# Kernel optimization log

Hardware: AMD Instinct MI355X
Metric: run time of the kernel (lower is better)

## Reference

```python
import jax, jax.numpy as jnp
import numpy as np

NUM_CLASSES = 80
STRIDES = (8, 16, 32)


def _decode(p, stride):
    # p: [B, 5+C, H, W] raw head -> [B, HW, 5+C] decoded (xy in px, wh=exp*stride)
    B, C, H, W = p.shape
    ys, xs = jnp.meshgrid(jnp.arange(H), jnp.arange(W), indexing='ij')
    grid = jnp.stack([xs, ys], -1).reshape(H * W, 2).astype(p.dtype)
    out = p.reshape(B, C, H * W).transpose(0, 2, 1)
    xy = (out[..., :2] + grid) * stride
    wh = jnp.exp(out[..., 2:4]) * stride
    out = jnp.concatenate([xy, wh, out[..., 4:]], -1)
    es = jnp.full((H * W,), float(stride), p.dtype)
    return out, grid[:, 0], grid[:, 1], es


def _pairwise_iou(gt, pr):
    # gt [G,4] cxcywh, pr [A,4] -> [G,A]
    gt_tl = gt[:, None, :2] - gt[:, None, 2:] * 0.5
    gt_br = gt[:, None, :2] + gt[:, None, 2:] * 0.5
    pr_tl = pr[None, :, :2] - pr[None, :, 2:] * 0.5
    pr_br = pr[None, :, :2] + pr[None, :, 2:] * 0.5
    tl = jnp.maximum(gt_tl, pr_tl)
    br = jnp.minimum(gt_br, pr_br)
    en = jnp.all(tl < br, -1).astype(gt.dtype)
    inter = jnp.prod(br - tl, -1) * en
    a_gt = jnp.prod(gt[:, 2:], -1)[:, None]
    a_pr = jnp.prod(pr[:, 2:], -1)[None, :]
    return inter / (a_gt + a_pr - inter + 1e-16)


def _assign(gt_boxes, gt_cls, bbox, clsp, objp, xg, yg, es):
    # SimOTA assignment for one image (all fixed-shape; non-candidate anchors
    # are masked out via huge cost instead of boolean gather).
    G = gt_boxes.shape[0]
    xc = (xg + 0.5) * es  # [A] anchor centers
    yc = (yg + 0.5) * es
    gl = gt_boxes[:, 0:1] - 0.5 * gt_boxes[:, 2:3]
    gr = gt_boxes[:, 0:1] + 0.5 * gt_boxes[:, 2:3]
    gt_ = gt_boxes[:, 1:2] - 0.5 * gt_boxes[:, 3:4]
    gb = gt_boxes[:, 1:2] + 0.5 * gt_boxes[:, 3:4]
    in_box = (xc[None] > gl) & (xc[None] < gr) & (yc[None] > gt_) & (yc[None] < gb)  # [G,A]
    r = 2.5 * es[None]
    in_ctr = ((xc[None] > gt_boxes[:, 0:1] - r) & (xc[None] < gt_boxes[:, 0:1] + r)
              & (yc[None] > gt_boxes[:, 1:2] - r) & (yc[None] < gt_boxes[:, 1:2] + r))
    fg_cand = jnp.any(in_box, 0) | jnp.any(in_ctr, 0)  # [A]
    in_both = in_box & in_ctr  # [G,A]

    ious = _pairwise_iou(gt_boxes, bbox)  # [G,A]
    ious_m = jnp.where(fg_cand[None, :], ious, 0.0)
    iou_cost = -jnp.log(ious_m + 1e-8)

    # pairwise cls BCE cost: bce(sqrt(sigmoid(cls)*sigmoid(obj)), onehot(gt)).sum(-1)
    p = jnp.sqrt(jax.nn.sigmoid(clsp) * jax.nn.sigmoid(objp[:, None]))  # [A,C]
    lp = jnp.maximum(jnp.log(p), -100.0)
    l1p = jnp.maximum(jnp.log1p(-p), -100.0)
    t = jax.nn.one_hot(gt_cls, NUM_CLASSES, dtype=p.dtype)  # [G,C]
    cls_cost = -(jnp.einsum('ac,gc->ga', lp - l1p, t) + jnp.sum(l1p, -1)[None, :])

    cost = (cls_cost + 3.0 * iou_cost
            + 1e5 * (~in_both).astype(p.dtype)
            + 1e9 * (~fg_cand)[None, :].astype(p.dtype))

    # dynamic-k: k_g = clamp(sum(top10 ious), min=1)
    topk_ious, _ = jax.lax.top_k(ious_m, 10)
    dyn_k = jnp.clip(topk_ious.sum(-1).astype(jnp.int32), 1, None)  # [G]
    rank = jnp.argsort(jnp.argsort(cost, axis=1), axis=1)  # rank of each anchor per gt
    matching = (rank < dyn_k[:, None]) & fg_cand[None, :]  # [G,A]
    # resolve anchors matched to multiple gts: keep min-cost gt
    multi = matching.sum(0) > 1
    best = jnp.argmin(cost, 0)
    matching = jnp.where(multi[None, :], jnp.arange(G)[:, None] == best[None, :], matching)

    fg = jnp.any(matching, 0)  # [A]
    matched_gt = jnp.argmax(matching, 0)  # [A]
    pred_iou = jnp.sum(matching * ious, 0)  # [A]
    matched_cls = gt_cls[matched_gt]
    return fg, matched_gt, pred_iou, matched_cls


def _giou_loss(b, g):
    tl = jnp.maximum(b[..., :2] - b[..., 2:] * 0.5, g[..., :2] - g[..., 2:] * 0.5)
    br = jnp.minimum(b[..., :2] + b[..., 2:] * 0.5, g[..., :2] + g[..., 2:] * 0.5)
    area_b = jnp.prod(b[..., 2:], -1)
    area_g = jnp.prod(g[..., 2:], -1)
    en = jnp.all(tl < br, -1).astype(b.dtype)
    inter = jnp.prod(br - tl, -1) * en
    union = area_b + area_g - inter
    iou = inter / (union + 1e-16)
    ctl = jnp.minimum(b[..., :2] - b[..., 2:] * 0.5, g[..., :2] - g[..., 2:] * 0.5)
    cbr = jnp.maximum(b[..., :2] + b[..., 2:] * 0.5, g[..., :2] + g[..., 2:] * 0.5)
    area_c = jnp.maximum(jnp.prod(cbr - ctl, -1), 1e-16)
    giou = iou - (area_c - union) / area_c
    return 1.0 - jnp.clip(giou, -1.0, 1.0)


def _bce_logits(x, t):
    return jnp.maximum(x, 0.0) - x * t + jnp.log1p(jnp.exp(-jnp.abs(x)))


def _forward(p8, p16, p32, labels):
    outs, xo, yo, eo = [], [], [], []
    for p, s in zip((p8, p16, p32), STRIDES):
        o, x, y, e = _decode(p, s)
        outs.append(o); xo.append(x); yo.append(y); eo.append(e)
    outputs = jnp.concatenate(outs, 1)  # [B, A, 5+C]
    xg = jnp.concatenate(xo); yg = jnp.concatenate(yo); es = jnp.concatenate(eo)

    bbox = outputs[..., :4]
    obj = outputs[..., 4]
    cls = outputs[..., 5:]
    gt_boxes = labels[..., :4]
    gt_cls = labels[..., 4].astype(jnp.int32)

    # assignment runs under no_grad in torch
    det = jax.lax.stop_gradient(outputs)
    fg, matched_gt, pred_iou, matched_cls = jax.vmap(
        lambda gb, gc, o: _assign(gb, gc, o[..., :4], o[..., 5:], o[..., 4], xg, yg, es)
    )(gt_boxes, gt_cls, det)

    fgf = fg.astype(outputs.dtype)  # [B,A]
    reg_t = jnp.take_along_axis(gt_boxes, matched_gt[..., None], axis=1)  # [B,A,4]
    cls_t = (jax.nn.one_hot(matched_cls, NUM_CLASSES, dtype=outputs.dtype)
             * pred_iou[..., None] * fgf[..., None])

    loss_iou = jnp.sum(_giou_loss(bbox, reg_t) * fgf)
    loss_obj = jnp.sum(_bce_logits(obj, fgf))
    loss_cls = jnp.sum(_bce_logits(cls, cls_t) * fgf[..., None])
    num_fg = jnp.maximum(jnp.sum(fgf), 1.0)
    return (5.0 * loss_iou + loss_obj + loss_cls) / num_fg


def setup_inputs() -> dict:
    key = jax.random.key(0)
    k1, k2, k3, k4, k5, k6 = jax.random.split(key, 6)
    B, NGT = 32, 20
    p8 = jax.random.normal(k1, (B, 5 + NUM_CLASSES, 80, 80), dtype=jnp.float32)
    p16 = jax.random.normal(k2, (B, 5 + NUM_CLASSES, 40, 40), dtype=jnp.float32)
    p32 = jax.random.normal(k3, (B, 5 + NUM_CLASSES, 20, 20), dtype=jnp.float32)
    cxy = jax.random.uniform(k4, (B, NGT, 2), dtype=jnp.float32, minval=32.0, maxval=608.0)
    wh = jax.random.uniform(k5, (B, NGT, 2), dtype=jnp.float32, minval=16.0, maxval=128.0)
    cls = jax.random.randint(k6, (B, NGT, 1), 0, NUM_CLASSES).astype(jnp.float32)
    labels = jnp.concatenate([cxy, wh, cls], -1)
    return {"p8": p8, "p16": p16, "p32": p32, "labels": labels}


def reference(p8, p16, p32, labels):
    return _forward(p8, p16, p32, labels)
```

## Files before the change

### kernel.cpp

```cpp
#include <hip/hip_runtime.h>
#include <cstdint>
#include <cstddef>

#define NA 8400
#define NAP 8448
#define NB 32
#define NG 20
#define NCL 80

__device__ __forceinline__ float frcp(float x) { return __builtin_amdgcn_rcpf(x); }
__device__ __forceinline__ float sigm(float x) { return frcp(1.0f + __expf(-x)); }
__device__ __forceinline__ float bce0(float x) {
  return fmaxf(x, 0.0f) + __logf(1.0f + __expf(-fabsf(x)));
}

__device__ __forceinline__ const float* anchor_base(const float* p8, const float* p16,
                                                    const float* p32, int b, int a,
                                                    int& hw, int& HW) {
  if (a < 6400)      { hw = a;        HW = 6400; return p8  + (size_t)b * 85 * 6400; }
  else if (a < 8000) { hw = a - 6400; HW = 1600; return p16 + (size_t)b * 85 * 1600; }
  hw = a - 8000; HW = 400; return p32 + (size_t)b * 85 * 400;
}

__device__ __forceinline__ float iou_raw(float gx, float gy, float gw, float gh, float4 p) {
  float gtlx = gx - gw * 0.5f, gtly = gy - gh * 0.5f;
  float gbrx = gx + gw * 0.5f, gbry = gy + gh * 0.5f;
  float ptlx = p.x - p.z * 0.5f, ptly = p.y - p.w * 0.5f;
  float pbrx = p.x + p.z * 0.5f, pbry = p.y + p.w * 0.5f;
  float tlx = fmaxf(gtlx, ptlx), tly = fmaxf(gtly, ptly);
  float brx = fminf(gbrx, pbrx), bry = fminf(gbry, pbry);
  float inter = ((tlx < brx) && (tly < bry)) ? (brx - tlx) * (bry - tly) : 0.0f;
  float ag = gw * gh, ap = p.z * p.w;
  return inter * frcp(ag + ap - inter + 1e-16f);
}

__device__ __forceinline__ float giou_loss(float4 bb, float gx, float gy, float gw, float gh) {
  float btlx = bb.x - bb.z * 0.5f, btly = bb.y - bb.w * 0.5f;
  float bbrx = bb.x + bb.z * 0.5f, bbry = bb.y + bb.w * 0.5f;
  float gtlx = gx - gw * 0.5f, gtly = gy - gh * 0.5f;
  float gbrx = gx + gw * 0.5f, gbry = gy + gh * 0.5f;
  float tlx = fmaxf(btlx, gtlx), tly = fmaxf(btly, gtly);
  float brx = fminf(bbrx, gbrx), bry = fminf(bbry, gbry);
  float area_b = bb.z * bb.w, area_g = gw * gh;
  float inter = ((tlx < brx) && (tly < bry)) ? (brx - tlx) * (bry - tly) : 0.0f;
  float uni = area_b + area_g - inter;
  float iou = inter / (uni + 1e-16f);
  float ctlx = fminf(btlx, gtlx), ctly = fminf(btly, gtly);
  float cbrx = fmaxf(bbrx, gbrx), cbry = fmaxf(bbry, gbry);
  float area_c = fmaxf((cbrx - ctlx) * (cbry - ctly), 1e-16f);
  float giou = iou - (area_c - uni) / area_c;
  giou = fminf(fmaxf(giou, -1.0f), 1.0f);
  return 1.0f - giou;
}

__device__ __forceinline__ void block_argmin(float& v, int& i, volatile float* s_v,
                                             volatile int* s_i, int tid) {
#pragma unroll
  for (int off = 32; off; off >>= 1) {
    float ov = __shfl_down(v, off, 64);
    int   oi = __shfl_down(i, off, 64);
    if (ov < v || (ov == v && oi < i)) { v = ov; i = oi; }
  }
  if ((tid & 63) == 0) { s_v[tid >> 6] = v; s_i[tid >> 6] = i; }
  __syncthreads();
  v = s_v[0]; i = s_i[0];
#pragma unroll
  for (int w = 1; w < 4; ++w) {
    float ov = s_v[w]; int oi = s_i[w];
    if (ov < v || (ov == v && oi < i)) { v = ov; i = oi; }
  }
}

__global__ __launch_bounds__(256) void kA(const float* __restrict__ p8,
                                          const float* __restrict__ p16,
                                          const float* __restrict__ p32,
                                          const float* __restrict__ labels,
                                          float4* __restrict__ bbox,
                                          float* __restrict__ sum_l1p,
                                          float* __restrict__ sum_bce0,
                                          float* __restrict__ w_tbl,
                                          unsigned int* __restrict__ amask,
                                          unsigned int* __restrict__ match_mask,
                                          float* __restrict__ accum) {
  __shared__ float s_gt[NG * 5];
  __shared__ unsigned int s_gmask[NCL];
  __shared__ float s_part[4];
  int b = blockIdx.y, tid = threadIdx.x;
  if (tid < NG * 5) s_gt[tid] = labels[(size_t)b * NG * 5 + tid];
  if (tid >= 128 && tid < 128 + NCL) s_gmask[tid - 128] = 0u;
  __syncthreads();
  if (tid < NG) { int c = (int)s_gt[tid * 5 + 4]; atomicOr(&s_gmask[c], 1u << tid); }
  __syncthreads();

  int a = blockIdx.x * 256 + tid;
  size_t ba = (size_t)b * NAP + a;
  match_mask[ba] = 0u;
  float bce_obj = 0.0f;
  if (a < NA) {
    int hw, HW, W, stride;
    const float* base;
    if (a < 6400)      { hw = a;        HW = 6400; W = 80; stride = 8;  base = p8  + (size_t)b * 85 * 6400; }
    else if (a < 8000) { hw = a - 6400; HW = 1600; W = 40; stride = 16; base = p16 + (size_t)b * 85 * 1600; }
    else               { hw = a - 8000; HW = 400;  W = 20; stride = 32; base = p32 + (size_t)b * 85 * 400;  }
    int xg = hw % W, yg = hw / W;
    float fs = (float)stride;

    float xc = ((float)xg + 0.5f) * fs;
    float yc = ((float)yg + 0.5f) * fs;
    float r = 2.5f * fs;
    unsigned int msk = 0u;
    bool fg = false;
#pragma unroll
    for (int g = 0; g < NG; ++g) {
      float gx = s_gt[g * 5 + 0], gy = s_gt[g * 5 + 1];
      float gw = s_gt[g * 5 + 2], gh = s_gt[g * 5 + 3];
      bool inb = (xc > gx - 0.5f * gw) && (xc < gx + 0.5f * gw) &&
                 (yc > gy - 0.5f * gh) && (yc < gy + 0.5f * gh);
      bool inc = (xc > gx - r) && (xc < gx + r) && (yc > gy - r) && (yc < gy + r);
      fg = fg || inb || inc;
      if (inb && inc) msk |= (1u << g);
    }
    if (fg) msk |= 0x80000000u;
    amask[ba] = msk;

    float obj = base[4 * HW + hw];
    float so = sigm(obj);
    bce_obj = bce0(obj);

    if (fg) {
      float v0 = base[hw];
      float v1 = base[HW + hw];
      float v2 = base[2 * HW + hw];
      float v3 = base[3 * HW + hw];
      bbox[ba] = make_float4((v0 + (float)xg) * fs, (v1 + (float)yg) * fs,
                             __expf(v2) * fs, __expf(v3) * fs);
      float sl = 0.0f, sb = 0.0f;
      for (int cc = 0; cc < NCL; cc += 8) {
        float xs[8];
#pragma unroll
        for (int j = 0; j < 8; ++j) xs[j] = base[(5 + cc + j) * HW + hw];
#pragma unroll
        for (int j = 0; j < 8; ++j) {
          float x = xs[j];
          float p = sqrtf(sigm(x) * so);
          float l1p = fmaxf(__logf(1.0f - p), -100.0f);
          sl += l1p;
          sb += bce0(x);
          unsigned int m = s_gmask[cc + j];
          if (m) {
            float w = fmaxf(__logf(p), -100.0f) - l1p;
            do {
              int g = __ffs(m) - 1; m &= m - 1;
              w_tbl[((size_t)b * NG + g) * NAP + a] = w;
            } while (m);
          }
        }
      }
      sum_l1p[ba] = sl;
      sum_bce0[ba] = sb;
    }
  } else {
    amask[ba] = 0u;
  }

#pragma unroll
  for (int off = 32; off; off >>= 1) bce_obj += __shfl_down(bce_obj, off, 64);
  if ((tid & 63) == 0) s_part[tid >> 6] = bce_obj;
  __syncthreads();
  if (tid == 0) atomicAdd(&accum[1], s_part[0] + s_part[1] + s_part[2] + s_part[3]);
}

__global__ __launch_bounds__(256) void kB(const float* __restrict__ labels,
                                          const float4* __restrict__ bbox,
                                          const float* __restrict__ sum_l1p,
                                          const float* __restrict__ w_tbl,
                                          const unsigned int* __restrict__ amask,
                                          unsigned int* __restrict__ match_mask) {
  __shared__ float s_cost[NAP];
  __shared__ float s_wt[4 * 10];
  __shared__ float s_v[4];
  __shared__ int   s_i[4];
  __shared__ int   s_k;

  int g = blockIdx.x, b = blockIdx.y, tid = threadIdx.x;
  int lane = tid & 63, wid = tid >> 6;
  size_t bA = (size_t)b * NAP;
  const float* __restrict__ wg = w_tbl + ((size_t)b * NG + g) * NAP;

  float gx = labels[(size_t)b * NG * 5 + g * 5 + 0];
  float gy = labels[(size_t)b * NG * 5 + g * 5 + 1];
  float gw = labels[(size_t)b * NG * 5 + g * 5 + 2];
  float gh = labels[(size_t)b * NG * 5 + g * 5 + 3];

  float t10[10];
#pragma unroll
  for (int j = 0; j < 10; ++j) t10[j] = 0.0f;

  for (int i0 = 0; i0 < 33; i0 += 3) {
    unsigned int am[3]; float wv[3], sl[3]; float4 pb[3];
#pragma unroll
    for (int j = 0; j < 3; ++j) {
      int a = tid + (i0 + j) * 256;
      am[j] = amask[bA + a];
      wv[j] = wg[a];
      sl[j] = sum_l1p[bA + a];
      pb[j] = bbox[bA + a];
    }
#pragma unroll
    for (int j = 0; j < 3; ++j) {
      int a = tid + (i0 + j) * 256;
      bool fg = (am[j] & 0x80000000u) != 0u;
      float iou = iou_raw(gx, gy, gw, gh, pb[j]);
      float ioum = fg ? iou : 0.0f;
      if (ioum > t10[9]) {
        t10[9] = ioum;
#pragma unroll
        for (int q = 9; q > 0; --q) {
          if (t10[q] > t10[q - 1]) { float t = t10[q]; t10[q] = t10[q - 1]; t10[q - 1] = t; }
          else break;
        }
      }
      float c = -(wv[j] + sl[j]) - 3.0f * __logf(ioum + 1e-8f);
      if (!((am[j] >> g) & 1u)) c += 100000.0f;
      if (!fg) c = 1e9f;
      s_cost[a] = c;
    }
  }

  for (int r = 0; r < 10; ++r) {
    float v = t10[0];
    float bv = v;
#pragma unroll
    for (int off = 32; off; off >>= 1) bv = fmaxf(bv, __shfl_down(bv, off, 64));
    bv = __shfl(bv, 0, 64);
    unsigned long long won = __ballot(v == bv);
    if (lane == __ffsll(won) - 1) {
#pragma unroll
      for (int q = 0; q < 9; ++q) t10[q] = t10[q + 1];
      t10[9] = -1.0f;
    }
    if (lane == 0) s_wt[wid * 10 + r] = bv;
  }
  __syncthreads();

  if (tid == 0) {
    int p0 = 0, p1 = 0, p2 = 0, p3 = 0;
    float s = 0.0f;
    for (int r = 0; r < 10; ++r) {
      float v0 = (p0 < 10) ? s_wt[p0]      : -2.0f;
      float v1 = (p1 < 10) ? s_wt[10 + p1] : -2.0f;
      float v2 = (p2 < 10) ? s_wt[20 + p2] : -2.0f;
      float v3 = (p3 < 10) ? s_wt[30 + p3] : -2.0f;
      float m01 = fmaxf(v0, v1), m23 = fmaxf(v2, v3);
      float m = fmaxf(m01, m23);
      s += m;
      if (m == v0) ++p0; else if (m == v1) ++p1; else if (m == v2) ++p2; else ++p3;
    }
    int k = (int)s;
    if (k < 1) k = 1;
    s_k = k;
  }
  __syncthreads();
  int k = s_k;

  for (int it = 0; it < k; ++it) {
    float bv = 3.4e38f; int bi = NAP;
    for (int a = tid; a < NAP; a += 256) {
      float v = s_cost[a];
      if (v < bv || (v == bv && a < bi)) { bv = v; bi = a; }
    }
    block_argmin(bv, bi, s_v, s_i, tid);
    if (bv >= 1e8f) break;
    if (tid == 0) {
      atomicOr(&match_mask[bA + bi], 1u << g);
      s_cost[bi] = 3.4e38f;
    }
    __syncthreads();
  }
}

__global__ __launch_bounds__(256) void kC(const float* __restrict__ p8,
                                          const float* __restrict__ p16,
                                          const float* __restrict__ p32,
                                          const float* __restrict__ labels,
                                          const float4* __restrict__ bbox,
                                          const float* __restrict__ sum_l1p,
                                          const float* __restrict__ sum_bce0,
                                          const float* __restrict__ w_tbl,
                                          const unsigned int* __restrict__ amask,
                                          const unsigned int* __restrict__ match_mask,
                                          float* __restrict__ accum) {
  __shared__ float s_gt[NG * 5];
  __shared__ float s_red[16];
  int b = blockIdx.y, tid = threadIdx.x;
  if (tid < NG * 5) s_gt[tid] = labels[(size_t)b * NG * 5 + tid];
  __syncthreads();

  int a = blockIdx.x * 256 + tid;
  size_t ba = (size_t)b * NAP + a;
  float li = 0.0f, oe = 0.0f, lc = 0.0f, nf = 0.0f;

  if (a < NA) {
    unsigned int m = match_mask[ba];
    if (m != 0u) {
      int hw, HW;
      const float* base = anchor_base(p8, p16, p32, b, a, hw, HW);
      float4 pb = bbox[ba];
      int mg;
      if (m & (m - 1)) {
        unsigned int am = amask[ba];
        float sl = sum_l1p[ba];
        float bestc = 3.4e38f; mg = 0;
#pragma unroll 4
        for (int g = 0; g < NG; ++g) {
          float iou = iou_raw(s_gt[g * 5], s_gt[g * 5 + 1], s_gt[g * 5 + 2], s_gt[g * 5 + 3], pb);
          float wv = w_tbl[((size_t)b * NG + g) * NAP + a];
          float c = -(wv + sl) - 3.0f * __logf(iou + 1e-8f);
          if (!((am >> g) & 1u)) c += 100000.0f;
          if (c < bestc) { bestc = c; mg = g; }
        }
      } else {
        mg = __ffs(m) - 1;
      }
      float gx = s_gt[mg * 5], gy = s_gt[mg * 5 + 1];
      float gw = s_gt[mg * 5 + 2], gh = s_gt[mg * 5 + 3];
      int cg = (int)s_gt[mg * 5 + 4];
      float piou = iou_raw(gx, gy, gw, gh, pb);
      li = giou_loss(pb, gx, gy, gw, gh);
      float xcls = base[(5 + cg) * HW + hw];
      lc = sum_bce0[ba] - xcls * piou;
      oe = base[4 * HW + hw];
      nf = 1.0f;
    }
  }

  float vals[4] = {li, oe, lc, nf};
#pragma unroll
  for (int q = 0; q < 4; ++q) {
#pragma unroll
    for (int off = 32; off; off >>= 1) vals[q] += __shfl_down(vals[q], off, 64);
  }
  if ((tid & 63) == 0) {
    int wid = tid >> 6;
    s_red[wid * 4 + 0] = vals[0];
    s_red[wid * 4 + 1] = vals[1];
    s_red[wid * 4 + 2] = vals[2];
    s_red[wid * 4 + 3] = vals[3];
  }
  __syncthreads();
  if (tid < 4) {
    const int slot[4] = {0, 2, 3, 4};
    float s = s_red[tid] + s_red[4 + tid] + s_red[8 + tid] + s_red[12 + tid];
    atomicAdd(&accum[slot[tid]], s);
  }
}

__global__ void kD(const float* __restrict__ accum, float* __restrict__ out) {
  float loss_iou = accum[0];
  float loss_obj = accum[1] - accum[2];
  float loss_cls = accum[3];
  float num_fg = fmaxf(accum[4], 1.0f);
  out[0] = (5.0f * loss_iou + loss_obj + loss_cls) / num_fg;
}

extern "C" void kernel_launch(void* const* d_in, const int* in_sizes, int n_in,
                              void* d_out, int out_size, void* d_ws, size_t ws_size,
                              hipStream_t stream) {
  const float* p8     = (const float*)d_in[0];
  const float* p16    = (const float*)d_in[1];
  const float* p32    = (const float*)d_in[2];
  const float* labels = (const float*)d_in[3];
  float* out = (float*)d_out;

  const size_t BAP = (size_t)NB * NAP;
  char* w = (char*)d_ws;
  float4*       bbox       = (float4*)w;
  unsigned int* match_mask = (unsigned int*)(w + BAP * 16);
  unsigned int* amask      = (unsigned int*)(w + BAP * 20);
  float*        sum_l1p    = (float*)(w + BAP * 24);
  float*        sum_bce0   = (float*)(w + BAP * 28);
  float*        w_tbl      = (float*)(w + BAP * 32);
  float*        accum      = (float*)(w + BAP * 32 + (size_t)NB * NG * NAP * 4);

  hipMemsetAsync(accum, 0, 32, stream);

  dim3 blk(256);
  kA<<<dim3(NAP / 256, NB), blk, 0, stream>>>(p8, p16, p32, labels, bbox, sum_l1p,
                                              sum_bce0, w_tbl, amask, match_mask, accum);
  kB<<<dim3(NG, NB), blk, 0, stream>>>(labels, bbox, sum_l1p, w_tbl, amask, match_mask);
  kC<<<dim3(NAP / 256, NB), blk, 0, stream>>>(p8, p16, p32, labels, bbox, sum_l1p,
                                              sum_bce0, w_tbl, amask, match_mask, accum);
  kD<<<1, 1, 0, stream>>>(accum, out);
}
```

Baseline: 204.9 us.

## Compact foreground anchors into per-image lists before cost and matching kernels

Splits the first kernel into a candidate pass, which uses ballot and prefix counts to build a compacted list of foreground anchors per image, and a class-cost pass that runs only over that list. The matching and loss kernels then iterate over compacted indices rather than all 8448 anchors, which cuts the argmin scans and global traffic on non-candidate anchors. The class-cost math is also rewritten in log-sigmoid form so one exp replaces the separate sigmoid and sqrt calls. In exchange the compaction kernel uses only one 1024-thread block per image with several barriers per iteration, which may serialize that stage.

Result: faster. 196.5 us (-4.1%).

```diff
diff --git a/kernel.cpp b/kernel.cpp
--- a/kernel.cpp
+++ b/kernel.cpp
@@ -9,17 +9,19 @@
 #define NCL 80
 
 __device__ __forceinline__ float frcp(float x) { return __builtin_amdgcn_rcpf(x); }
-__device__ __forceinline__ float sigm(float x) { return frcp(1.0f + __expf(-x)); }
 __device__ __forceinline__ float bce0(float x) {
   return fmaxf(x, 0.0f) + __logf(1.0f + __expf(-fabsf(x)));
 }
 
-__device__ __forceinline__ const float* anchor_base(const float* p8, const float* p16,
-                                                    const float* p32, int b, int a,
-                                                    int& hw, int& HW) {
-  if (a < 6400)      { hw = a;        HW = 6400; return p8  + (size_t)b * 85 * 6400; }
-  else if (a < 8000) { hw = a - 6400; HW = 1600; return p16 + (size_t)b * 85 * 1600; }
-  hw = a - 8000; HW = 400; return p32 + (size_t)b * 85 * 400;
+__device__ __forceinline__ void anchor_info(int a, const float* p8, const float* p16,
+                                            const float* p32, int b, const float*& base,
+                                            int& hw, int& HW, int& xg, int& yg, float& fs) {
+  if (a < 6400)      { hw = a;        HW = 6400; xg = hw % 80; yg = hw / 80; fs = 8.f;
+                       base = p8  + (size_t)b * 85 * 6400; }
+  else if (a < 8000) { hw = a - 6400; HW = 1600; xg = hw % 40; yg = hw / 40; fs = 16.f;
+                       base = p16 + (size_t)b * 85 * 1600; }
+  else               { hw = a - 8000; HW = 400;  xg = hw % 20; yg = hw / 20; fs = 32.f;
+                       base = p32 + (size_t)b * 85 * 400; }
 }
 
 __device__ __forceinline__ float iou_raw(float gx, float gy, float gw, float gh, float4 p) {
@@ -71,111 +73,159 @@
   }
 }
 
-__global__ __launch_bounds__(256) void kA(const float* __restrict__ p8,
-                                          const float* __restrict__ p16,
-                                          const float* __restrict__ p32,
-                                          const float* __restrict__ labels,
-                                          float4* __restrict__ bbox,
-                                          float* __restrict__ sum_l1p,
-                                          float* __restrict__ sum_bce0,
-                                          float* __restrict__ w_tbl,
-                                          unsigned int* __restrict__ amask,
-                                          unsigned int* __restrict__ match_mask,
-                                          float* __restrict__ accum) {
-  __shared__ float s_gt[NG * 5];
-  __shared__ unsigned int s_gmask[NCL];
-  __shared__ float s_part[4];
-  int b = blockIdx.y, tid = threadIdx.x;
-  if (tid < NG * 5) s_gt[tid] = labels[(size_t)b * NG * 5 + tid];
-  if (tid >= 128 && tid < 128 + NCL) s_gmask[tid - 128] = 0u;
-  __syncthreads();
-  if (tid < NG) { int c = (int)s_gt[tid * 5 + 4]; atomicOr(&s_gmask[c], 1u << tid); }
-  __syncthreads();
-
-  int a = blockIdx.x * 256 + tid;
-  size_t ba = (size_t)b * NAP + a;
-  match_mask[ba] = 0u;
+__global__ __launch_bounds__(1024) void kA0(const float* __restrict__ p8,
+                                            const float* __restrict__ p16,
+                                            const float* __restrict__ p32,
+                                            const float* __restrict__ labels,
+                                            unsigned int* __restrict__ am_c,
+                                            int* __restrict__ fg_list,
+                                            int* __restrict__ n_fg,
+                                            unsigned int* __restrict__ match_c,
+                                            float* __restrict__ accum) {
+  __shared__ float s_gt[NG * 4];
+  __shared__ unsigned int s_wcnt[16];
+  __shared__ unsigned int s_base;
+  __shared__ float s_part[16];
+  int b = blockIdx.x, tid = threadIdx.x, lane = tid & 63, wid = tid >> 6;
+  if (tid < NG) {
+    s_gt[tid * 4 + 0] = labels[((size_t)b * NG + tid) * 5 + 0];
+    s_gt[tid * 4 + 1] = labels[((size_t)b * NG + tid) * 5 + 1];
+    s_gt[tid * 4 + 2] = labels[((size_t)b * NG + tid) * 5 + 2];
+    s_gt[tid * 4 + 3] = labels[((size_t)b * NG + tid) * 5 + 3];
+  }
+  if (tid == 0) s_base = 0u;
+  __syncthreads();
+
   float bce_obj = 0.0f;
-  if (a < NA) {
-    int hw, HW, W, stride;
-    const float* base;
-    if (a < 6400)      { hw = a;        HW = 6400; W = 80; stride = 8;  base = p8  + (size_t)b * 85 * 6400; }
-    else if (a < 8000) { hw = a - 6400; HW = 1600; W = 40; stride = 16; base = p16 + (size_t)b * 85 * 1600; }
-    else               { hw = a - 8000; HW = 400;  W = 20; stride = 32; base = p32 + (size_t)b * 85 * 400;  }
-    int xg = hw % W, yg = hw / W;
-    float fs = (float)stride;
-
-    float xc = ((float)xg + 0.5f) * fs;
-    float yc = ((float)yg + 0.5f) * fs;
-    float r = 2.5f * fs;
+  for (int it = 0; it < 9; ++it) {
+    int a = it * 1024 + tid;
     unsigned int msk = 0u;
     bool fg = false;
-#pragma unroll
-    for (int g = 0; g < NG; ++g) {
-      float gx = s_gt[g * 5 + 0], gy = s_gt[g * 5 + 1];
-      float gw = s_gt[g * 5 + 2], gh = s_gt[g * 5 + 3];
-      bool inb = (xc > gx - 0.5f * gw) && (xc < gx + 0.5f * gw) &&
-                 (yc > gy - 0.5f * gh) && (yc < gy + 0.5f * gh);
-      bool inc = (xc > gx - r) && (xc < gx + r) && (yc > gy - r) && (yc < gy + r);
-      fg = fg || inb || inc;
-      if (inb && inc) msk |= (1u << g);
-    }
-    if (fg) msk |= 0x80000000u;
-    amask[ba] = msk;
+    if (a < NA) {
+      const float* base; int hw, HW, xg, yg; float fs;
+      anchor_info(a, p8, p16, p32, b, base, hw, HW, xg, yg, fs);
+      float obj = base[4 * HW + hw];
+      bce_obj += bce0(obj);
+      float xc = ((float)xg + 0.5f) * fs;
+      float yc = ((float)yg + 0.5f) * fs;
+      float r = 2.5f * fs;
+#pragma unroll
+      for (int g = 0; g < NG; ++g) {
+        float gx = s_gt[g * 4 + 0], gy = s_gt[g * 4 + 1];
+        float gw = s_gt[g * 4 + 2], gh = s_gt[g * 4 + 3];
+        bool inb = (xc > gx - 0.5f * gw) && (xc < gx + 0.5f * gw) &&
+                   (yc > gy - 0.5f * gh) && (yc < gy + 0.5f * gh);
+        bool inc = (xc > gx - r) && (xc < gx + r) && (yc > gy - r) && (yc < gy + r);
+        fg = fg || inb || inc;
+        if (inb && inc) msk |= (1u << g);
+      }
+    }
+    if (a < NAP) match_c[(size_t)b * NAP + a] = 0u;
+
+    unsigned long long bm = __ballot(fg);
+    if (lane == 0) s_wcnt[wid] = (unsigned int)__popcll(bm);
+    __syncthreads();
+    unsigned int pos = s_base;
+    for (int w = 0; w < wid; ++w) pos += s_wcnt[w];
+    if (fg) {
+      pos += (unsigned int)__popcll(bm & ((1ull << lane) - 1ull));
+      fg_list[(size_t)b * NAP + pos] = a;
+      am_c[(size_t)b * NAP + pos] = msk | 0x80000000u;
+    }
+    __syncthreads();
+    if (tid == 0) {
+      unsigned int t = 0;
+      for (int w = 0; w < 16; ++w) t += s_wcnt[w];
+      s_base += t;
+    }
+    __syncthreads();
+  }
+  if (tid == 0) n_fg[b] = (int)s_base;
+
+#pragma unroll
+  for (int off = 32; off; off >>= 1) bce_obj += __shfl_down(bce_obj, off, 64);
+  if (lane == 0) s_part[wid] = bce_obj;
+  __syncthreads();
+  if (tid == 0) {
+    float t = 0.0f;
+    for (int w = 0; w < 16; ++w) t += s_part[w];
+    atomicAdd(&accum[1], t);
+  }
+}
+
+__global__ __launch_bounds__(256) void kA1(const float* __restrict__ p8,
+                                           const float* __restrict__ p16,
+                                           const float* __restrict__ p32,
+                                           const float* __restrict__ labels,
+                                           const int* __restrict__ fg_list,
+                                           const int* __restrict__ n_fg,
+                                           float4* __restrict__ bbox_c,
+                                           float* __restrict__ sl_c,
+                                           float* __restrict__ sb_c,
+                                           float* __restrict__ w_c) {
+  __shared__ unsigned int s_gmask[NCL];
+  int b = blockIdx.y, tid = threadIdx.x;
+  if (tid < NCL) s_gmask[tid] = 0u;
+  __syncthreads();
+  if (tid < NG) {
+    int c = (int)labels[((size_t)b * NG + tid) * 5 + 4];
+    atomicOr(&s_gmask[c], 1u << tid);
+  }
+  __syncthreads();
+
+  int n = n_fg[b];
+  for (int ci = blockIdx.x * 256 + tid; ci < n; ci += gridDim.x * 256) {
+    int a = fg_list[(size_t)b * NAP + ci];
+    const float* base; int hw, HW, xg, yg; float fs;
+    anchor_info(a, p8, p16, p32, b, base, hw, HW, xg, yg, fs);
 
     float obj = base[4 * HW + hw];
-    float so = sigm(obj);
-    bce_obj = bce0(obj);
-
-    if (fg) {
-      float v0 = base[hw];
-      float v1 = base[HW + hw];
-      float v2 = base[2 * HW + hw];
-      float v3 = base[3 * HW + hw];
-      bbox[ba] = make_float4((v0 + (float)xg) * fs, (v1 + (float)yg) * fs,
-                             __expf(v2) * fs, __expf(v3) * fs);
-      float sl = 0.0f, sb = 0.0f;
-      for (int cc = 0; cc < NCL; cc += 8) {
-        float xs[8];
-#pragma unroll
-        for (int j = 0; j < 8; ++j) xs[j] = base[(5 + cc + j) * HW + hw];
-#pragma unroll
-        for (int j = 0; j < 8; ++j) {
-          float x = xs[j];
-          float p = sqrtf(sigm(x) * so);
-          float l1p = fmaxf(__logf(1.0f - p), -100.0f);
-          sl += l1p;
-          sb += bce0(x);
-          unsigned int m = s_gmask[cc + j];
-          if (m) {
-            float w = fmaxf(__logf(p), -100.0f) - l1p;
-            do {
-              int g = __ffs(m) - 1; m &= m - 1;
-              w_tbl[((size_t)b * NG + g) * NAP + a] = w;
-            } while (m);
-          }
+    float v0 = base[hw];
+    float v1 = base[HW + hw];
+    float v2 = base[2 * HW + hw];
+    float v3 = base[3 * HW + hw];
+    bbox_c[(size_t)b * NAP + ci] = make_float4((v0 + (float)xg) * fs, (v1 + (float)yg) * fs,
+                                               __expf(v2) * fs, __expf(v3) * fs);
+    float uo  = __logf(1.0f + __expf(-fabsf(obj)));
+    float lso = fminf(obj, 0.0f) - uo;
+
+    float sl = 0.0f, sb = 0.0f;
+    for (int cc = 0; cc < NCL; cc += 8) {
+      float xs[8];
+#pragma unroll
+      for (int j = 0; j < 8; ++j) xs[j] = base[(5 + cc + j) * HW + hw];
+#pragma unroll
+      for (int j = 0; j < 8; ++j) {
+        float x = xs[j];
+        float u = __logf(1.0f + __expf(-fabsf(x)));
+        sb += fmaxf(x, 0.0f) + u;
+        float lsx = fminf(x, 0.0f) - u;
+        float lpr = 0.5f * (lsx + lso);
+        float p   = __expf(lpr);
+        float l1p = fmaxf(__logf(1.0f - p), -100.0f);
+        sl += l1p;
+        unsigned int m = s_gmask[cc + j];
+        if (m) {
+          float w = fmaxf(lpr, -100.0f) - l1p;
+          do {
+            int g = __ffs(m) - 1; m &= m - 1;
+            w_c[((size_t)b * NG + g) * NAP + ci] = w;
+          } while (m);
         }
       }
-      sum_l1p[ba] = sl;
-      sum_bce0[ba] = sb;
-    }
-  } else {
-    amask[ba] = 0u;
-  }
-
-#pragma unroll
-  for (int off = 32; off; off >>= 1) bce_obj += __shfl_down(bce_obj, off, 64);
-  if ((tid & 63) == 0) s_part[tid >> 6] = bce_obj;
-  __syncthreads();
-  if (tid == 0) atomicAdd(&accum[1], s_part[0] + s_part[1] + s_part[2] + s_part[3]);
+    }
+    sl_c[(size_t)b * NAP + ci] = sl;
+    sb_c[(size_t)b * NAP + ci] = sb;
+  }
 }
 
 __global__ __launch_bounds__(256) void kB(const float* __restrict__ labels,
-                                          const float4* __restrict__ bbox,
-                                          const float* __restrict__ sum_l1p,
-                                          const float* __restrict__ w_tbl,
-                                          const unsigned int* __restrict__ amask,
-                                          unsigned int* __restrict__ match_mask) {
+                                          const float4* __restrict__ bbox_c,
+                                          const float* __restrict__ sl_c,
+                                          const float* __restrict__ w_c,
+                                          const unsigned int* __restrict__ am_c,
+                                          const int* __restrict__ n_fg,
+                                          unsigned int* __restrict__ match_c) {
   __shared__ float s_cost[NAP];
   __shared__ float s_wt[4 * 10];
   __shared__ float s_v[4];
@@ -184,47 +234,36 @@
 
   int g = blockIdx.x, b = blockIdx.y, tid = threadIdx.x;
   int lane = tid & 63, wid = tid >> 6;
-  size_t bA = (size_t)b * NAP;
-  const float* __restrict__ wg = w_tbl + ((size_t)b * NG + g) * NAP;
-
-  float gx = labels[(size_t)b * NG * 5 + g * 5 + 0];
-  float gy = labels[(size_t)b * NG * 5 + g * 5 + 1];
-  float gw = labels[(size_t)b * NG * 5 + g * 5 + 2];
-  float gh = labels[(size_t)b * NG * 5 + g * 5 + 3];
+  int n = n_fg[b];
+  size_t bo = (size_t)b * NAP;
+  const float* __restrict__ wg = w_c + ((size_t)b * NG + g) * NAP;
+
+  float gx = labels[((size_t)b * NG + g) * 5 + 0];
+  float gy = labels[((size_t)b * NG + g) * 5 + 1];
+  float gw = labels[((size_t)b * NG + g) * 5 + 2];
+  float gh = labels[((size_t)b * NG + g) * 5 + 3];
 
   float t10[10];
 #pragma unroll
   for (int j = 0; j < 10; ++j) t10[j] = 0.0f;
 
-  for (int i0 = 0; i0 < 33; i0 += 3) {
-    unsigned int am[3]; float wv[3], sl[3]; float4 pb[3];
-#pragma unroll
-    for (int j = 0; j < 3; ++j) {
-      int a = tid + (i0 + j) * 256;
-      am[j] = amask[bA + a];
-      wv[j] = wg[a];
-      sl[j] = sum_l1p[bA + a];
-      pb[j] = bbox[bA + a];
-    }
-#pragma unroll
-    for (int j = 0; j < 3; ++j) {
-      int a = tid + (i0 + j) * 256;
-      bool fg = (am[j] & 0x80000000u) != 0u;
-      float iou = iou_raw(gx, gy, gw, gh, pb[j]);
-      float ioum = fg ? iou : 0.0f;
-      if (ioum > t10[9]) {
-        t10[9] = ioum;
-#pragma unroll
-        for (int q = 9; q > 0; --q) {
-          if (t10[q] > t10[q - 1]) { float t = t10[q]; t10[q] = t10[q - 1]; t10[q - 1] = t; }
-          else break;
-        }
+  for (int ci = tid; ci < n; ci += 256) {
+    unsigned int am = am_c[bo + ci];
+    float wv = wg[ci];
+    float sl = sl_c[bo + ci];
+    float4 pb = bbox_c[bo + ci];
+    float iou = iou_raw(gx, gy, gw, gh, pb);
+    if (iou > t10[9]) {
+      t10[9] = iou;
+#pragma unroll
+      for (int q = 9; q > 0; --q) {
+        if (t10[q] > t10[q - 1]) { float t = t10[q]; t10[q] = t10[q - 1]; t10[q - 1] = t; }
+        else break;
       }
-      float c = -(wv[j] + sl[j]) - 3.0f * __logf(ioum + 1e-8f);
-      if (!((am[j] >> g) & 1u)) c += 100000.0f;
-      if (!fg) c = 1e9f;
-      s_cost[a] = c;
-    }
+    }
+    float c = -(wv + sl) - 3.0f * __logf(iou + 1e-8f);
+    if (!((am >> g) & 1u)) c += 100000.0f;
+    s_cost[ci] = c;
   }
 
   for (int r = 0; r < 10; ++r) {
@@ -251,8 +290,7 @@
       float v1 = (p1 < 10) ? s_wt[10 + p1] : -2.0f;
       float v2 = (p2 < 10) ? s_wt[20 + p2] : -2.0f;
       float v3 = (p3 < 10) ? s_wt[30 + p3] : -2.0f;
-      float m01 = fmaxf(v0, v1), m23 = fmaxf(v2, v3);
-      float m = fmaxf(m01, m23);
+      float m = fmaxf(fmaxf(v0, v1), fmaxf(v2, v3));
       s += m;
       if (m == v0) ++p0; else if (m == v1) ++p1; else if (m == v2) ++p2; else ++p3;
     }
@@ -265,14 +303,14 @@
 
   for (int it = 0; it < k; ++it) {
     float bv = 3.4e38f; int bi = NAP;
-    for (int a = tid; a < NAP; a += 256) {
-      float v = s_cost[a];
-      if (v < bv || (v == bv && a < bi)) { bv = v; bi = a; }
+    for (int ci = tid; ci < n; ci += 256) {
+      float v = s_cost[ci];
+      if (v < bv || (v == bv && ci < bi)) { bv = v; bi = ci; }
     }
     block_argmin(bv, bi, s_v, s_i, tid);
     if (bv >= 1e8f) break;
     if (tid == 0) {
-      atomicOr(&match_mask[bA + bi], 1u << g);
+      atomicOr(&match_c[bo + bi], 1u << g);
       s_cost[bi] = 3.4e38f;
     }
     __syncthreads();
@@ -283,12 +321,14 @@
                                           const float* __restrict__ p16,
                                           const float* __restrict__ p32,
                                           const float* __restrict__ labels,
-                                          const float4* __restrict__ bbox,
-                                          const float* __restrict__ sum_l1p,
-                                          const float* __restrict__ sum_bce0,
-                                          const float* __restrict__ w_tbl,
-                                          const unsigned int* __restrict__ amask,
-                                          const unsigned int* __restrict__ match_mask,
+                                          const float4* __restrict__ bbox_c,
+                                          const float* __restrict__ sl_c,
+                                          const float* __restrict__ sb_c,
+                                          const float* __restrict__ w_c,
+                                          const unsigned int* __restrict__ am_c,
+                                          const int* __restrict__ fg_list,
+                                          const int* __restrict__ n_fg,
+                                          const unsigned int* __restrict__ match_c,
                                           float* __restrict__ accum) {
   __shared__ float s_gt[NG * 5];
   __shared__ float s_red[16];
@@ -296,42 +336,42 @@
   if (tid < NG * 5) s_gt[tid] = labels[(size_t)b * NG * 5 + tid];
   __syncthreads();
 
-  int a = blockIdx.x * 256 + tid;
-  size_t ba = (size_t)b * NAP + a;
+  int n = n_fg[b];
+  size_t bo = (size_t)b * NAP;
   float li = 0.0f, oe = 0.0f, lc = 0.0f, nf = 0.0f;
 
-  if (a < NA) {
-    unsigned int m = match_mask[ba];
-    if (m != 0u) {
-      int hw, HW;
-      const float* base = anchor_base(p8, p16, p32, b, a, hw, HW);
-      float4 pb = bbox[ba];
-      int mg;
-      if (m & (m - 1)) {
-        unsigned int am = amask[ba];
-        float sl = sum_l1p[ba];
-        float bestc = 3.4e38f; mg = 0;
+  for (int ci = blockIdx.x * 256 + tid; ci < n; ci += gridDim.x * 256) {
+    unsigned int m = match_c[bo + ci];
+    if (m == 0u) continue;
+    int a = fg_list[bo + ci];
+    const float* base; int hw, HW, xg, yg; float fs;
+    anchor_info(a, p8, p16, p32, b, base, hw, HW, xg, yg, fs);
+    float4 pb = bbox_c[bo + ci];
+    int mg;
+    if (m & (m - 1)) {
+      unsigned int am = am_c[bo + ci];
+      float sl = sl_c[bo + ci];
+      float bestc = 3.4e38f; mg = 0;
 #pragma unroll 4
-        for (int g = 0; g < NG; ++g) {
-          float iou = iou_raw(s_gt[g * 5], s_gt[g * 5 + 1], s_gt[g * 5 + 2], s_gt[g * 5 + 3], pb);
-          float wv = w_tbl[((size_t)b * NG + g) * NAP + a];
-          float c = -(wv + sl) - 3.0f * __logf(iou + 1e-8f);
-          if (!((am >> g) & 1u)) c += 100000.0f;
-          if (c < bestc) { bestc = c; mg = g; }
-        }
-      } else {
-        mg = __ffs(m) - 1;
+      for (int g = 0; g < NG; ++g) {
+        float iou = iou_raw(s_gt[g * 5], s_gt[g * 5 + 1], s_gt[g * 5 + 2], s_gt[g * 5 + 3], pb);
+        float wv = w_c[((size_t)b * NG + g) * NAP + ci];
+        float c = -(wv + sl) - 3.0f * __logf(iou + 1e-8f);
+        if (!((am >> g) & 1u)) c += 100000.0f;
+        if (c < bestc) { bestc = c; mg = g; }
       }
-      float gx = s_gt[mg * 5], gy = s_gt[mg * 5 + 1];
-      float gw = s_gt[mg * 5 + 2], gh = s_gt[mg * 5 + 3];
-      int cg = (int)s_gt[mg * 5 + 4];
-      float piou = iou_raw(gx, gy, gw, gh, pb);
-      li = giou_loss(pb, gx, gy, gw, gh);
-      float xcls = base[(5 + cg) * HW + hw];
-      lc = sum_bce0[ba] - xcls * piou;
-      oe = base[4 * HW + hw];
-      nf = 1.0f;
-    }
+    } else {
+      mg = __ffs(m) - 1;
+    }
+    float gx = s_gt[mg * 5], gy = s_gt[mg * 5 + 1];
+    float gw = s_gt[mg * 5 + 2], gh = s_gt[mg * 5 + 3];
+    int cg = (int)s_gt[mg * 5 + 4];
+    float piou = iou_raw(gx, gy, gw, gh, pb);
+    li += giou_loss(pb, gx, gy, gw, gh);
+    float xcls = base[(5 + cg) * HW + hw];
+    lc += sb_c[bo + ci] - xcls * piou;
+    oe += base[4 * HW + hw];
+    nf += 1.0f;
   }
 
   float vals[4] = {li, oe, lc, nf};
@@ -374,21 +414,25 @@
 
   const size_t BAP = (size_t)NB * NAP;
   char* w = (char*)d_ws;
-  float4*       bbox       = (float4*)w;
-  unsigned int* match_mask = (unsigned int*)(w + BAP * 16);
-  unsigned int* amask      = (unsigned int*)(w + BAP * 20);
-  float*        sum_l1p    = (float*)(w + BAP * 24);
-  float*        sum_bce0   = (float*)(w + BAP * 28);
-  float*        w_tbl      = (float*)(w + BAP * 32);
-  float*        accum      = (float*)(w + BAP * 32 + (size_t)NB * NG * NAP * 4);
+  float4*       bbox_c  = (float4*)w;
+  float*        w_c     = (float*)(w + BAP * 16);
+  char*         w2      = w + BAP * 16 + (size_t)NB * NG * NAP * 4;
+  int*          fg_list = (int*)(w2);
+  unsigned int* am_c    = (unsigned int*)(w2 + BAP * 4);
+  unsigned int* match_c = (unsigned int*)(w2 + BAP * 8);
+  float*        sl_c    = (float*)(w2 + BAP * 12);
+  float*        sb_c    = (float*)(w2 + BAP * 16);
+  int*          n_fg    = (int*)(w2 + BAP * 20);
+  float*        accum   = (float*)(w2 + BAP * 20 + 128);
 
   hipMemsetAsync(accum, 0, 32, stream);
 
-  dim3 blk(256);
-  kA<<<dim3(NAP / 256, NB), blk, 0, stream>>>(p8, p16, p32, labels, bbox, sum_l1p,
-                                              sum_bce0, w_tbl, amask, match_mask, accum);
-  kB<<<dim3(NG, NB), blk, 0, stream>>>(labels, bbox, sum_l1p, w_tbl, amask, match_mask);
-  kC<<<dim3(NAP / 256, NB), blk, 0, stream>>>(p8, p16, p32, labels, bbox, sum_l1p,
-                                              sum_bce0, w_tbl, amask, match_mask, accum);
+  kA0<<<dim3(NB), dim3(1024), 0, stream>>>(p8, p16, p32, labels, am_c, fg_list, n_fg,
+                                           match_c, accum);
+  kA1<<<dim3(12, NB), dim3(256), 0, stream>>>(p8, p16, p32, labels, fg_list, n_fg,
+                                              bbox_c, sl_c, sb_c, w_c);
+  kB<<<dim3(NG, NB), dim3(256), 0, stream>>>(labels, bbox_c, sl_c, w_c, am_c, n_fg, match_c);
+  kC<<<dim3(12, NB), dim3(256), 0, stream>>>(p8, p16, p32, labels, bbox_c, sl_c, sb_c, w_c,
+                                             am_c, fg_list, n_fg, match_c, accum);
   kD<<<1, 1, 0, stream>>>(accum, out);
 }
```
